# Kernel tuning notes

Measured on AMD Instinct MI355X. Metric: run time of the kernel, lower is better.

## Reference

```python
import jax, jax.numpy as jnp
import numpy as np

B, T, C, H, NC = 512, 256, 512, 512, 96  # batch, encoder steps, channels, hidden, num classes


def setup_inputs() -> dict:
    key = jax.random.key(0)
    ks = jax.random.split(key, 12)
    def w(k, shape, fan):
        return (jax.random.normal(k, shape, jnp.float32) / np.sqrt(fan)).astype(jnp.float32)
    labels = jax.random.randint(ks[0], (B,), 0, NC)
    return {
        "prev_h": jax.random.normal(ks[1], (B, H), jnp.float32),
        "prev_c": jax.random.normal(ks[2], (B, H), jnp.float32),
        "batch_H": jax.random.normal(ks[3], (B, T, C), jnp.float32),
        "char_onehots": jax.nn.one_hot(labels, NC, dtype=jnp.float32),
        "Wi": w(ks[4], (C, H), C),            # i2h kernel (no bias)
        "Wh": w(ks[5], (H, H), H),            # h2h kernel
        "bh": jnp.zeros((H,), jnp.float32),    # h2h bias
        "Ws": w(ks[6], (H, 1), H),            # score kernel (no bias)
        "K": w(ks[7], (C + NC, 4 * H), C + NC),  # LSTM input kernel (i,f,g,o)
        "R": w(ks[8], (H, 4 * H), H),            # LSTM recurrent kernel
        "b": jnp.zeros((4 * H,), jnp.float32),    # LSTM bias
    }


def reference(prev_h, prev_c, batch_H, char_onehots, Wi, Wh, bh, Ws, K, R, b):
    # Additive (Bahdanau) attention
    proj = jnp.einsum('btc,ch->bth', batch_H, Wi)                  # [B,T,H]
    hp = prev_h @ Wh + bh                                          # [B,H]
    e = jnp.einsum('bth,h->bt', jnp.tanh(proj + hp[:, None, :]), Ws[:, 0])  # [B,T]
    alpha = jax.nn.softmax(e, axis=1)                              # [B,T]
    context = jnp.einsum('bt,btc->bc', alpha, batch_H)             # [B,C]
    # LSTMCell step (keras gate order: i, f, g, o; sigmoid recurrent act, tanh act)
    x = jnp.concatenate([context, char_onehots], axis=1)           # [B,C+NC]
    z = x @ K + prev_h @ R + b                                     # [B,4H]
    i, f, g, o = jnp.split(z, 4, axis=1)
    c_new = jax.nn.sigmoid(f) * prev_c + jax.nn.sigmoid(i) * jnp.tanh(g)
    h_new = jax.nn.sigmoid(o) * jnp.tanh(c_new)
    return (h_new, c_new, alpha[:, :, None])  # ((h,c), alpha[B,T,1])
```

## Files before the change

kernel.cpp:

```cpp
#include <hip/hip_runtime.h>
#include <hip/hip_bf16.h>
#include <stdint.h>

#define KFULL 1120
#define N4H   2048
#define MTOT  131072

typedef float f32x4 __attribute__((ext_vector_type(4)));
typedef __bf16 bf16x8 __attribute__((ext_vector_type(8)));
typedef unsigned short u16;
typedef unsigned short ush8 __attribute__((ext_vector_type(8)));

__device__ __forceinline__ u16 f2bf(float f){
  union { float f; unsigned u; } v; v.f = f;
  unsigned u = v.u;
  u += 0x7fffu + ((u >> 16) & 1u);
  return (u16)(u >> 16);
}
__device__ __forceinline__ float sigf(float x){ return 1.f / (1.f + __expf(-x)); }
__device__ __forceinline__ float tanh_fast(float x){ return 1.f - 2.f / (__expf(2.f * x) + 1.f); }
__device__ __forceinline__ int swz(int row){ return (row ^ (row >> 2)) & 3; }

__global__ void prep_w(const float* __restrict__ Wi, const float* __restrict__ Wh,
                       const float* __restrict__ Km, const float* __restrict__ R,
                       u16* __restrict__ wiT, u16* __restrict__ whT, u16* __restrict__ wfT){
  int idx = blockIdx.x * 256 + threadIdx.x;
  if (idx < 524288){
    const float* src = (idx < 262144) ? Wi : Wh;
    u16* dst = (idx < 262144) ? wiT : whT;
    int e = idx & 262143;
    int n = e & 511, kk = (e >> 9) & 31, s = e >> 14;
    float v = src[(size_t)(s * 32 + kk) * 512 + n];
    int dkk = (kk & 7) | ((((kk >> 3) ^ swz(n)) & 3) << 3);
    dst[((size_t)s * 512 + n) * 32 + dkk] = f2bf(v);
  } else {
    int e = idx - 524288;
    if (e >= 35 * 2048 * 32) return;
    int n = e & 2047, kk = (e >> 11) & 31, s = e >> 16;
    int k = s * 32 + kk;
    float v = (k < 608) ? Km[(size_t)k * 2048 + n] : R[(size_t)(k - 608) * 2048 + n];
    int dkk = (kk & 7) | ((((kk >> 3) ^ swz(n)) & 3) << 3);
    wfT[((size_t)s * 2048 + n) * 32 + dkk] = f2bf(v);
  }
}

__global__ void prep_x(const float* __restrict__ onehots, const float* __restrict__ prev_h,
                       float* __restrict__ x_full){
  int idx = blockIdx.x * 256 + threadIdx.x;
  if (idx >= 512 * 608) return;
  int b = idx / 608, c = idx % 608;
  float v = (c < 96) ? onehots[b * 96 + c] : prev_h[b * 512 + (c - 96)];
  x_full[(size_t)b * KFULL + 512 + c] = v;
}

template<int EPI>
__launch_bounds__(256, 3)
__global__ void gemm128(const float* __restrict__ A, int lda, int ksteps,
                        const u16* __restrict__ Bt, int ntot,
                        float* __restrict__ outp, size_t partStride,
                        const float* __restrict__ hpart, const float* __restrict__ bh,
                        const float* __restrict__ Ws, float* __restrict__ epart){
  __shared__ u16 smA[128 * 32];
  __shared__ u16 smB[128 * 32];
  __shared__ float smHp[128];
  __shared__ float smWs[128];
  __shared__ float smRed[2][128];

  const int tid  = threadIdx.x;
  const int lane = tid & 63, w = tid >> 6;
  const int wr = w >> 1, wc = w & 1;
  const int fr = lane & 15, g = lane >> 4;

  int m0, n0, s0;
  if (EPI == 1){
    int bid = blockIdx.x;
    int sw = (bid & 7) * 512 + (bid >> 3);
    m0 = (sw >> 2) * 128;
    n0 = (sw & 3) * 128;
    s0 = 0;
  } else {
    m0 = blockIdx.x * 128;
    n0 = blockIdx.y * 128;
    s0 = blockIdx.z * ksteps;
    outp += (size_t)blockIdx.z * partStride;
  }

  if (EPI == 1 && tid < 128){
    int b = m0 >> 8;
    float h = bh[n0 + tid];
    #pragma unroll
    for (int p = 0; p < 4; ++p) h += hpart[(size_t)p * 262144 + (size_t)b * 512 + n0 + tid];
    smHp[tid] = h;
    smWs[tid] = Ws[n0 + tid];
  }

  f32x4 acc[4][4] = {};

  const int ar = tid >> 2;
  const int ac = (tid & 3) * 8;
  const float* ap = A + (size_t)(m0 + ar) * lda + ac;
  const int sz  = swz(ar);
  const int ab0 = ar * 64 + (((tid & 3) ^ sz) << 4);
  const int ab1 = ab0 + 64 * 64;

  for (int s = 0; s < ksteps; ++s){
    const int kc = (s0 + s) * 32;
    const char* bsrc = (const char*)Bt + ((size_t)(s0 + s) * ntot + n0) * 64;
    #pragma unroll
    for (int j = 0; j < 2; ++j){
      int off = w * 2048 + j * 1024;
      __builtin_amdgcn_global_load_lds(
        (const __attribute__((address_space(1))) void*)(bsrc + off + lane * 16),
        (__attribute__((address_space(3))) void*)((char*)smB + off),
        16, 0, 0);
    }
    float4 a0 = *(const float4*)(ap + kc);
    float4 a1 = *(const float4*)(ap + kc + 4);
    float4 a2 = *(const float4*)(ap + (size_t)64 * lda + kc);
    float4 a3 = *(const float4*)(ap + (size_t)64 * lda + kc + 4);
    ush8 w0, w1;
    w0[0]=f2bf(a0.x); w0[1]=f2bf(a0.y); w0[2]=f2bf(a0.z); w0[3]=f2bf(a0.w);
    w0[4]=f2bf(a1.x); w0[5]=f2bf(a1.y); w0[6]=f2bf(a1.z); w0[7]=f2bf(a1.w);
    w1[0]=f2bf(a2.x); w1[1]=f2bf(a2.y); w1[2]=f2bf(a2.z); w1[3]=f2bf(a2.w);
    w1[4]=f2bf(a3.x); w1[5]=f2bf(a3.y); w1[6]=f2bf(a3.z); w1[7]=f2bf(a3.w);
    *(ush8*)((char*)smA + ab0) = w0;
    *(ush8*)((char*)smA + ab1) = w1;
    __syncthreads();

    bf16x8 af[4];
    #pragma unroll
    for (int m = 0; m < 4; ++m){
      int rl = wr * 64 + m * 16 + fr;
      af[m] = *(const bf16x8*)((const char*)smA + rl * 64 + ((g ^ swz(rl)) << 4));
    }
    #pragma unroll
    for (int n = 0; n < 4; ++n){
      int nl = wc * 64 + n * 16 + fr;
      bf16x8 bfv = *(const bf16x8*)((const char*)smB + nl * 64 + ((g ^ swz(nl)) << 4));
      #pragma unroll
      for (int m = 0; m < 4; ++m)
        acc[m][n] = __builtin_amdgcn_mfma_f32_16x16x32_bf16(af[m], bfv, acc[m][n], 0, 0, 0);
    }
    __syncthreads();
  }

  if (EPI == 0){
    #pragma unroll
    for (int n = 0; n < 4; ++n){
      int col = n0 + wc * 64 + n * 16 + fr;
      #pragma unroll
      for (int m = 0; m < 4; ++m){
        int row = m0 + wr * 64 + m * 16 + g * 4;
        #pragma unroll
        for (int j = 0; j < 4; ++j)
          outp[(size_t)(row + j) * ntot + col] = acc[m][n][j];
      }
    }
  } else {
    float p[16] = {};
    #pragma unroll
    for (int n = 0; n < 4; ++n){
      int col = wc * 64 + n * 16 + fr;
      float hpv = smHp[col], wsv = smWs[col];
      #pragma unroll
      for (int m = 0; m < 4; ++m)
        #pragma unroll
        for (int j = 0; j < 4; ++j)
          p[m * 4 + j] += tanh_fast(acc[m][n][j] + hpv) * wsv;
    }
    #pragma unroll
    for (int mask = 1; mask < 16; mask <<= 1)
      #pragma unroll
      for (int i = 0; i < 16; ++i)
        p[i] += __shfl_xor(p[i], mask);
    if (fr == 0){
      #pragma unroll
      for (int m = 0; m < 4; ++m)
        #pragma unroll
        for (int j = 0; j < 4; ++j)
          smRed[wc][wr * 64 + m * 16 + g * 4 + j] = p[m * 4 + j];
    }
    __syncthreads();
    if (tid < 128){
      int nb = n0 >> 7;
      epart[(size_t)nb * MTOT + m0 + tid] = smRed[0][tid] + smRed[1][tid];
    }
  }
}

__global__ void ctx_softmax(const float* __restrict__ epart, const float* __restrict__ batch_H,
                            float* __restrict__ x_full, float* __restrict__ alpha_out){
  __shared__ float sa[256];
  __shared__ float red[4], red2[4];
  __shared__ f32x4 sred[8][32];
  int b = blockIdx.x, q = blockIdx.y, tid = threadIdx.x;

  float e = 0.f;
  #pragma unroll
  for (int p = 0; p < 4; ++p) e += epart[(size_t)p * MTOT + b * 256 + tid];
  float m = e;
  #pragma unroll
  for (int mask = 1; mask < 64; mask <<= 1) m = fmaxf(m, __shfl_xor(m, mask));
  int w = tid >> 6;
  if ((tid & 63) == 0) red[w] = m;
  __syncthreads();
  m = fmaxf(fmaxf(red[0], red[1]), fmaxf(red[2], red[3]));
  float ev = __expf(e - m);
  float s = ev;
  #pragma unroll
  for (int mask = 1; mask < 64; mask <<= 1) s += __shfl_xor(s, mask);
  if ((tid & 63) == 0) red2[w] = s;
  __syncthreads();
  s = red2[0] + red2[1] + red2[2] + red2[3];
  float a = ev / s;
  sa[tid] = a;
  if (q == 0) alpha_out[(size_t)b * 256 + tid] = a;
  __syncthreads();

  int c4 = tid & 31, tq = tid >> 5;
  const float4* bhp = (const float4*)(batch_H + (size_t)b * 131072) + (size_t)tq * 32 * 128 + q * 32 + c4;
  f32x4 acc = {0.f, 0.f, 0.f, 0.f};
  #pragma unroll 4
  for (int t = 0; t < 32; ++t){
    float av = sa[tq * 32 + t];
    float4 v = bhp[(size_t)t * 128];
    acc[0] += av * v.x; acc[1] += av * v.y; acc[2] += av * v.z; acc[3] += av * v.w;
  }
  sred[tq][c4] = acc;
  __syncthreads();
  if (tid < 32){
    f32x4 o = sred[0][tid];
    #pragma unroll
    for (int r = 1; r < 8; ++r){
      f32x4 v = sred[r][tid];
      o[0] += v[0]; o[1] += v[1]; o[2] += v[2]; o[3] += v[3];
    }
    float4 st; st.x = o[0]; st.y = o[1]; st.z = o[2]; st.w = o[3];
    *(float4*)(x_full + (size_t)b * KFULL + q * 128 + tid * 4) = st;
  }
}

__global__ void gates_k(const float* __restrict__ zpart, const float* __restrict__ bias,
                        const float* __restrict__ prev_c, float* __restrict__ out){
  int idx = blockIdx.x * 256 + threadIdx.x;
  int b = idx >> 9, h = idx & 511;
  float zi = bias[h], zf = bias[512 + h], zg = bias[1024 + h], zo = bias[1536 + h];
  #pragma unroll
  for (int p = 0; p < 5; ++p){
    const float* zr = zpart + (size_t)p * 1048576 + (size_t)b * N4H;
    zi += zr[h]; zf += zr[512 + h]; zg += zr[1024 + h]; zo += zr[1536 + h];
  }
  float c = sigf(zf) * prev_c[idx] + sigf(zi) * tanh_fast(zg);
  float hn = sigf(zo) * tanh_fast(c);
  out[idx] = hn;
  out[262144 + idx] = c;
}

extern "C" void kernel_launch(void* const* d_in, const int* in_sizes, int n_in,
                              void* d_out, int out_size, void* d_ws, size_t ws_size,
                              hipStream_t stream){
  const float* prev_h  = (const float*)d_in[0];
  const float* prev_c  = (const float*)d_in[1];
  const float* batch_H = (const float*)d_in[2];
  const float* onehots = (const float*)d_in[3];
  const float* Wi      = (const float*)d_in[4];
  const float* Wh      = (const float*)d_in[5];
  const float* bh      = (const float*)d_in[6];
  const float* Ws      = (const float*)d_in[7];
  const float* Km      = (const float*)d_in[8];
  const float* R       = (const float*)d_in[9];
  const float* bb      = (const float*)d_in[10];
  float* out = (float*)d_out;

  char* ws = (char*)d_ws;
  u16*  wiT    = (u16*)(ws + 0);
  u16*  whT    = (u16*)(ws + 524288);
  u16*  wfT    = (u16*)(ws + 1048576);
  float* hpart = (float*)(ws + 5636096);
  float* epart = (float*)(ws + 9830400);
  float* x_full= (float*)(ws + 11927552);
  float* zpart = (float*)(ws + 14221312);

  float* alpha = out + 524288;

  prep_w<<<11008, 256, 0, stream>>>(Wi, Wh, Km, R, wiT, whT, wfT);
  prep_x<<<1216, 256, 0, stream>>>(onehots, prev_h, x_full);
  gemm128<0><<<dim3(4, 4, 4), 256, 0, stream>>>(prev_h, 512, 4, whT, 512,
                                                hpart, 262144, nullptr, nullptr, nullptr, nullptr);
  gemm128<1><<<dim3(4096, 1, 1), 256, 0, stream>>>(batch_H, 512, 16, wiT, 512,
                                                   nullptr, 0, hpart, bh, Ws, epart);
  ctx_softmax<<<dim3(512, 4), 256, 0, stream>>>(epart, batch_H, x_full, alpha);
  gemm128<0><<<dim3(4, 16, 5), 256, 0, stream>>>(x_full, KFULL, 7, wfT, N4H,
                                                 zpart, 1048576, nullptr, nullptr, nullptr, nullptr);
  gates_k<<<1024, 256, 0, stream>>>(zpart, bb, prev_c, out);
}
```

Measured before the change: 207.9 us.

## Double-buffer LDS tiles in gemm128 to overlap global loads with MFMA

```diff
diff --git a/kernel.cpp b/kernel.cpp
--- a/kernel.cpp
+++ b/kernel.cpp
@@ -60,8 +60,8 @@
                         float* __restrict__ outp, size_t partStride,
                         const float* __restrict__ hpart, const float* __restrict__ bh,
                         const float* __restrict__ Ws, float* __restrict__ epart){
-  __shared__ u16 smA[128 * 32];
-  __shared__ u16 smB[128 * 32];
+  __shared__ u16 smA[2][128 * 32];
+  __shared__ u16 smB[2][128 * 32];
   __shared__ float smHp[128];
   __shared__ float smWs[128];
   __shared__ float smRed[2][128];
@@ -103,46 +103,75 @@
   const int ab0 = ar * 64 + (((tid & 3) ^ sz) << 4);
   const int ab1 = ab0 + 64 * 64;
 
-  for (int s = 0; s < ksteps; ++s){
-    const int kc = (s0 + s) * 32;
-    const char* bsrc = (const char*)Bt + ((size_t)(s0 + s) * ntot + n0) * 64;
-    #pragma unroll
-    for (int j = 0; j < 2; ++j){
-      int off = w * 2048 + j * 1024;
-      __builtin_amdgcn_global_load_lds(
-        (const __attribute__((address_space(1))) void*)(bsrc + off + lane * 16),
-        (__attribute__((address_space(3))) void*)((char*)smB + off),
-        16, 0, 0);
-    }
-    float4 a0 = *(const float4*)(ap + kc);
-    float4 a1 = *(const float4*)(ap + kc + 4);
-    float4 a2 = *(const float4*)(ap + (size_t)64 * lda + kc);
-    float4 a3 = *(const float4*)(ap + (size_t)64 * lda + kc + 4);
-    ush8 w0, w1;
-    w0[0]=f2bf(a0.x); w0[1]=f2bf(a0.y); w0[2]=f2bf(a0.z); w0[3]=f2bf(a0.w);
-    w0[4]=f2bf(a1.x); w0[5]=f2bf(a1.y); w0[6]=f2bf(a1.z); w0[7]=f2bf(a1.w);
-    w1[0]=f2bf(a2.x); w1[1]=f2bf(a2.y); w1[2]=f2bf(a2.z); w1[3]=f2bf(a2.w);
-    w1[4]=f2bf(a3.x); w1[5]=f2bf(a3.y); w1[6]=f2bf(a3.z); w1[7]=f2bf(a3.w);
-    *(ush8*)((char*)smA + ab0) = w0;
-    *(ush8*)((char*)smA + ab1) = w1;
+  float4 a0, a1, a2, a3;
+
+#define ISSUE_B(sabs, c) do {                                              \
+    const char* bsrc = (const char*)Bt + ((size_t)(sabs) * ntot + n0) * 64;\
+    _Pragma("unroll")                                                      \
+    for (int j = 0; j < 2; ++j){                                           \
+      int off = w * 2048 + j * 1024;                                       \
+      __builtin_amdgcn_global_load_lds(                                    \
+        (const __attribute__((address_space(1))) void*)(bsrc + off + lane * 16), \
+        (__attribute__((address_space(3))) void*)((char*)&smB[c][0] + off),\
+        16, 0, 0);                                                         \
+    }                                                                      \
+  } while(0)
+
+#define LOAD_A(s) do {                                                     \
+    int kc = (s0 + (s)) * 32;                                              \
+    a0 = *(const float4*)(ap + kc);                                        \
+    a1 = *(const float4*)(ap + kc + 4);                                    \
+    a2 = *(const float4*)(ap + (size_t)64 * lda + kc);                     \
+    a3 = *(const float4*)(ap + (size_t)64 * lda + kc + 4);                 \
+  } while(0)
+
+#define WRITE_A(c) do {                                                    \
+    ush8 w0, w1;                                                           \
+    w0[0]=f2bf(a0.x); w0[1]=f2bf(a0.y); w0[2]=f2bf(a0.z); w0[3]=f2bf(a0.w);\
+    w0[4]=f2bf(a1.x); w0[5]=f2bf(a1.y); w0[6]=f2bf(a1.z); w0[7]=f2bf(a1.w);\
+    w1[0]=f2bf(a2.x); w1[1]=f2bf(a2.y); w1[2]=f2bf(a2.z); w1[3]=f2bf(a2.w);\
+    w1[4]=f2bf(a3.x); w1[5]=f2bf(a3.y); w1[6]=f2bf(a3.z); w1[7]=f2bf(a3.w);\
+    *(ush8*)((char*)&smA[c][0] + ab0) = w0;                                \
+    *(ush8*)((char*)&smA[c][0] + ab1) = w1;                                \
+  } while(0)
+
+#define COMPUTE(c) do {                                                    \
+    bf16x8 af[4];                                                          \
+    _Pragma("unroll")                                                      \
+    for (int m = 0; m < 4; ++m){                                           \
+      int rl = wr * 64 + m * 16 + fr;                                      \
+      af[m] = *(const bf16x8*)((const char*)&smA[c][0] + rl * 64 + ((g ^ swz(rl)) << 4)); \
+    }                                                                      \
+    _Pragma("unroll")                                                      \
+    for (int n = 0; n < 4; ++n){                                           \
+      int nl = wc * 64 + n * 16 + fr;                                      \
+      bf16x8 bfv = *(const bf16x8*)((const char*)&smB[c][0] + nl * 64 + ((g ^ swz(nl)) << 4)); \
+      _Pragma("unroll")                                                    \
+      for (int m = 0; m < 4; ++m)                                          \
+        acc[m][n] = __builtin_amdgcn_mfma_f32_16x16x32_bf16(af[m], bfv, acc[m][n], 0, 0, 0); \
+    }                                                                      \
+  } while(0)
+
+  ISSUE_B(s0, 0);
+  LOAD_A(0);
+  WRITE_A(0);
+  __syncthreads();
+
+  int c = 0;
+  for (int s = 0; s < ksteps - 1; ++s){
+    ISSUE_B(s0 + s + 1, c ^ 1);
+    LOAD_A(s + 1);
+    COMPUTE(c);
+    WRITE_A(c ^ 1);
     __syncthreads();
-
-    bf16x8 af[4];
-    #pragma unroll
-    for (int m = 0; m < 4; ++m){
-      int rl = wr * 64 + m * 16 + fr;
-      af[m] = *(const bf16x8*)((const char*)smA + rl * 64 + ((g ^ swz(rl)) << 4));
-    }
-    #pragma unroll
-    for (int n = 0; n < 4; ++n){
-      int nl = wc * 64 + n * 16 + fr;
-      bf16x8 bfv = *(const bf16x8*)((const char*)smB + nl * 64 + ((g ^ swz(nl)) << 4));
-      #pragma unroll
-      for (int m = 0; m < 4; ++m)
-        acc[m][n] = __builtin_amdgcn_mfma_f32_16x16x32_bf16(af[m], bfv, acc[m][n], 0, 0, 0);
-    }
-    __syncthreads();
-  }
+    c ^= 1;
+  }
+  COMPUTE(c);
+
+#undef ISSUE_B
+#undef LOAD_A
+#undef WRITE_A
+#undef COMPUTE
 
   if (EPI == 0){
     #pragma unroll
@@ -173,6 +202,7 @@
       #pragma unroll
       for (int i = 0; i < 16; ++i)
         p[i] += __shfl_xor(p[i], mask);
+    __syncthreads();
     if (fr == 0){
       #pragma unroll
       for (int m = 0; m < 4; ++m)
```

After: 232.7 us. 1.12x slower.
